# Performance work log

Hardware: AMD Instinct MI355X
Metric: run time of the kernel (lower is better)

The kernel has to match this reference:

```python
import jax, jax.numpy as jnp
import numpy as np

# Static complete 8-ary label tree, depth 4, BFS (heap) indexing:
# children of node j are 8j+1..8j+8; level d starts at (8^d - 1)/7.
BRANCH = 8
DEPTH = 4
COUNTS = [BRANCH ** d for d in range(DEPTH + 1)]   # [1, 8, 64, 512, 4096]
STARTS = np.cumsum([0] + COUNTS)[:-1]              # level start offsets
N = int(sum(COUNTS))                               # 4681 nodes
B = 64
IN_DIM = 256
MEM = 256


def setup_inputs() -> dict:
    key = jax.random.key(0)
    ks = jax.random.split(key, 8)
    def w(k, shape, fan):
        return jax.random.normal(k, shape, jnp.float32) / np.float32(np.sqrt(fan))
    return {
        "inputs": jax.random.normal(ks[0], (N, B, IN_DIM), jnp.float32),
        "prob": jax.random.uniform(ks[1], (N, N), dtype=jnp.float32),
        "Wioux": w(ks[2], (3 * MEM, IN_DIM), IN_DIM),
        "bioux": jnp.zeros((3 * MEM,), jnp.float32),
        "Wiouh": w(ks[3], (3 * MEM, MEM), MEM),
        "biouh": jnp.zeros((3 * MEM,), jnp.float32),
        "Wfx": w(ks[4], (MEM, IN_DIM), IN_DIM),
        "bfx": jnp.zeros((MEM,), jnp.float32),
        "Wfh": w(ks[5], (MEM, MEM), MEM),
        "bfh": jnp.zeros((MEM,), jnp.float32),
    }


def _linear(x, W, b):
    # torch nn.Linear: y = x @ W^T + b
    return jnp.einsum("...i,oi->...o", x, W) + b


def reference(inputs, prob, Wioux, bioux, Wiouh, biouh, Wfx, bfx, Wfh, bfh):
    # --- leaf level (deepest): child_c = child_h = 0, but iouh/fh biases still apply
    s, cnt = int(STARTS[DEPTH]), COUNTS[DEPTH]
    x = inputs[s:s + cnt]                              # [nL, B, IN]
    iou = _linear(x, Wioux, bioux) + biouh             # iouh(0) = its bias
    i, o, u = jnp.split(iou, 3, axis=-1)
    c = jax.nn.sigmoid(i) * jnp.tanh(u)                # sum(f*0) = 0 for leaves
    h = jax.nn.sigmoid(o) * jnp.tanh(c)                # [nL, B, MEM]
    # --- internal levels, bottom-up (level-synchronous == original recursion)
    for d in range(DEPTH - 1, -1, -1):
        s, cnt = int(STARTS[d]), COUNTS[d]
        parents = jnp.arange(s, s + cnt)                                   # [cnt]
        childs = BRANCH * parents[:, None] + 1 + jnp.arange(BRANCH)[None]  # [cnt,8]
        pw = prob[parents[:, None], childs]                                # [cnt,8]
        wc = pw[:, :, None, None] * c.reshape(cnt, BRANCH, B, MEM)         # weighted child_c
        wh = pw[:, :, None, None] * h.reshape(cnt, BRANCH, B, MEM)         # weighted child_h
        h_sum = wh.sum(axis=1)                                             # [cnt,B,MEM]
        x = inputs[s:s + cnt]                                              # [cnt,B,IN]
        iou = _linear(x, Wioux, bioux) + _linear(h_sum, Wiouh, biouh)
        i, o, u = jnp.split(iou, 3, axis=-1)
        f = jax.nn.sigmoid(_linear(wh, Wfh, bfh) + _linear(x, Wfx, bfx)[:, None])
        c = jax.nn.sigmoid(i) * jnp.tanh(u) + (f * wc).sum(axis=1)
        h = jax.nn.sigmoid(o) * jnp.tanh(c)
    # root bottom_up_state: (c, h), each [B, MEM]
    return c[0], h[0]
```

## Files before the change

kernel.cpp:

```cpp
#include <hip/hip_runtime.h>


typedef unsigned short u16;
typedef unsigned int u32;
typedef __bf16 bf16x8 __attribute__((ext_vector_type(8)));
typedef float f32x4 __attribute__((ext_vector_type(4)));

#define STR 72
#define NNODES 4681

__device__ __forceinline__ float bf2f(u32 lo) { return __uint_as_float(lo << 16); }
__device__ __forceinline__ u16 f2bf(float f) {
    __bf16 h = (__bf16)f;
    return *(u16*)&h;
}
__device__ __forceinline__ float rcp_(float x) { return __builtin_amdgcn_rcpf(x); }
__device__ __forceinline__ float sigm(float x) { return rcp_(1.0f + __expf(-x)); }
__device__ __forceinline__ float tanh_(float x) {
    float e = __expf(2.0f * x);
    return 1.0f - 2.0f * rcp_(e + 1.0f);
}

__device__ __forceinline__ void stage_bf16(u16* lds, const u16* src, int tid) {
    int row = tid >> 2, c = (tid & 3) * 16;
    const u16* p = src + (size_t)row * 256 + c;
    uint4 v0 = *(const uint4*)p;
    uint4 v1 = *(const uint4*)(p + 8);
    u16* q = lds + row * STR + c;
    *(uint4*)q = v0;
    *(uint4*)(q + 8) = v1;
}
__device__ __forceinline__ void stage_f32(u16* lds, const float* src, int tid) {
    int row = tid >> 2, c = (tid & 3) * 16;
    const float* p = src + (size_t)row * 256 + c;
    u16 pk[16];
#pragma unroll
    for (int q = 0; q < 4; q++) {
        float4 v = *(const float4*)(p + q * 4);
        pk[q * 4 + 0] = f2bf(v.x);
        pk[q * 4 + 1] = f2bf(v.y);
        pk[q * 4 + 2] = f2bf(v.z);
        pk[q * 4 + 3] = f2bf(v.w);
    }
    u16* q2 = lds + row * STR + c;
    *(uint4*)q2 = *(uint4*)pk;
    *(uint4*)(q2 + 8) = *(uint4*)(pk + 8);
}

template <int NG>
__device__ __forceinline__ void mma_ksub(const u16* As, const u16* Ws, int wv, int l,
                                         int s, f32x4 (*acc)[4]) {
    const int colb = l & 15, quad = l >> 4;
    const int ko = s * 32 + quad * 8;
    bf16x8 a[4];
#pragma unroll
    for (int r = 0; r < 4; r++)
        a[r] = *(const bf16x8*)(As + (r * 16 + colb) * STR + ko);
#pragma unroll
    for (int g = 0; g < NG; g++) {
        bf16x8 b = *(const bf16x8*)(Ws + g * (64 * STR) + (wv * 16 + colb) * STR + ko);
#pragma unroll
        for (int r = 0; r < 4; r++)
            acc[g][r] = __builtin_amdgcn_mfma_f32_16x16x32_bf16(a[r], b, acc[g][r], 0, 0, 0);
    }
}

__global__ __launch_bounds__(256) void k_cvtw(
    const float* __restrict__ Wioux, const float* __restrict__ Wiouh,
    const float* __restrict__ Wfx, const float* __restrict__ Wfh,
    u16* __restrict__ out) {
    int i4 = (blockIdx.x * 256 + threadIdx.x) * 4;
    const float* p;
    if (i4 < 196608) p = Wioux + i4;
    else if (i4 < 393216) p = Wiouh + (i4 - 196608);
    else if (i4 < 458752) p = Wfx + (i4 - 393216);
    else p = Wfh + (i4 - 458752);
    float4 v = *(const float4*)p;
    u16 pk[4] = {f2bf(v.x), f2bf(v.y), f2bf(v.z), f2bf(v.w)};
    *(ushort4*)(out + i4) = *(ushort4*)pk;
}

__global__ __launch_bounds__(256) void k_leaf(
    const float* __restrict__ X, const u16* __restrict__ Wxb,
    const float* __restrict__ bioux, const float* __restrict__ biouh,
    u16* __restrict__ Cp, u16* __restrict__ Hp) {
    __shared__ u16 As[64 * STR];
    __shared__ u16 Ws[3][64 * STR];
    const int tid = threadIdx.x;
    const int mem0 = blockIdx.x * 64;
    const int row0 = blockIdx.y * 64;
    const int l = tid & 63, wv = tid >> 6;
    f32x4 acc[3][4];
#pragma unroll
    for (int g = 0; g < 3; g++)
#pragma unroll
        for (int r = 0; r < 4; r++) acc[g][r] = (f32x4){0.f, 0.f, 0.f, 0.f};
    for (int kt = 0; kt < 256; kt += 64) {
        stage_f32(As, X + (size_t)row0 * 256 + kt, tid);
#pragma unroll
        for (int g = 0; g < 3; g++)
            stage_bf16(Ws[g], Wxb + ((size_t)g * 256 + mem0) * 256 + kt, tid);
        __syncthreads();
        mma_ksub<3>(As, &Ws[0][0], wv, l, 0, acc);
        mma_ksub<3>(As, &Ws[0][0], wv, l, 1, acc);
        __syncthreads();
    }
    const int colb = l & 15, quad = l >> 4;
    const int mem = mem0 + wv * 16 + colb;
    const float bi = bioux[mem] + biouh[mem];
    const float bo = bioux[256 + mem] + biouh[256 + mem];
    const float bu = bioux[512 + mem] + biouh[512 + mem];
#pragma unroll
    for (int r = 0; r < 4; r++)
#pragma unroll
        for (int reg = 0; reg < 4; reg++) {
            int row = row0 + r * 16 + quad * 4 + reg;
            float c = sigm(acc[0][r][reg] + bi) * tanh_(acc[2][r][reg] + bu);
            float h = sigm(acc[1][r][reg] + bo) * tanh_(c);
            size_t o = (size_t)row * 256 + mem;
            Cp[o] = f2bf(c);
            Hp[o] = f2bf(h);
        }
}

__global__ __launch_bounds__(256) void k_g(
    const u16* Hprev, const u16* __restrict__ Wfhb, u16* Gout) {
    __shared__ u16 As[64 * STR];
    __shared__ u16 Ws[4][64 * STR];
    const int tid = threadIdx.x;
    const int row0 = blockIdx.x * 64;
    const int l = tid & 63, wv = tid >> 6;
    f32x4 acc[4][4];
#pragma unroll
    for (int g = 0; g < 4; g++)
#pragma unroll
        for (int r = 0; r < 4; r++) acc[g][r] = (f32x4){0.f, 0.f, 0.f, 0.f};
    for (int kt = 0; kt < 256; kt += 64) {
        stage_bf16(As, Hprev + (size_t)row0 * 256 + kt, tid);
#pragma unroll
        for (int g = 0; g < 4; g++)
            stage_bf16(Ws[g], Wfhb + ((size_t)g * 64) * 256 + kt, tid);
        __syncthreads();
        mma_ksub<4>(As, &Ws[0][0], wv, l, 0, acc);
        mma_ksub<4>(As, &Ws[0][0], wv, l, 1, acc);
        __syncthreads();
    }
    const int colb = l & 15, quad = l >> 4;
#pragma unroll
    for (int g = 0; g < 4; g++)
#pragma unroll
        for (int r = 0; r < 4; r++) {
            int n = g * 64 + wv * 16 + colb;
#pragma unroll
            for (int reg = 0; reg < 4; reg++) {
                int row = row0 + r * 16 + quad * 4 + reg;
                Gout[(size_t)row * 256 + n] = f2bf(acc[g][r][reg]);
            }
        }
}

__global__ __launch_bounds__(256) void k_main(
    const float* __restrict__ X, const u16* __restrict__ Hsum,
    const u16* __restrict__ G, const u16* __restrict__ Cprev,
    const float* __restrict__ pw,
    const u16* __restrict__ Wxb, const float* __restrict__ bioux,
    const u16* __restrict__ Whb, const float* __restrict__ biouh,
    const u16* __restrict__ Wfxb, const float* __restrict__ bfx,
    const float* __restrict__ bfh,
    u16* __restrict__ Ccur, u16* __restrict__ Hcur,
    float* __restrict__ outc, float* __restrict__ outh) {
    __shared__ u16 As[64 * STR];
    __shared__ u16 Ws[4][64 * STR];
    __shared__ float pws[8];
    const int tid = threadIdx.x;
    const int mem0 = blockIdx.x * 64;
    const int lp = blockIdx.y;
    const int l = tid & 63, wv = tid >> 6;
    if (tid < 8) pws[tid] = pw[lp * 8 + tid];
    f32x4 acc[4][4];
#pragma unroll
    for (int g = 0; g < 4; g++)
#pragma unroll
        for (int r = 0; r < 4; r++) acc[g][r] = (f32x4){0.f, 0.f, 0.f, 0.f};
    for (int kt = 0; kt < 256; kt += 64) {
        stage_f32(As, X + ((size_t)lp * 64) * 256 + kt, tid);
#pragma unroll
        for (int g = 0; g < 3; g++)
            stage_bf16(Ws[g], Wxb + ((size_t)g * 256 + mem0) * 256 + kt, tid);
        stage_bf16(Ws[3], Wfxb + (size_t)mem0 * 256 + kt, tid);
        __syncthreads();
        mma_ksub<4>(As, &Ws[0][0], wv, l, 0, acc);
        mma_ksub<4>(As, &Ws[0][0], wv, l, 1, acc);
        __syncthreads();
    }
    for (int kt = 0; kt < 256; kt += 64) {
        stage_bf16(As, Hsum + ((size_t)lp * 64) * 256 + kt, tid);
#pragma unroll
        for (int g = 0; g < 3; g++)
            stage_bf16(Ws[g], Whb + ((size_t)g * 256 + mem0) * 256 + kt, tid);
        __syncthreads();
        mma_ksub<3>(As, &Ws[0][0], wv, l, 0, acc);
        mma_ksub<3>(As, &Ws[0][0], wv, l, 1, acc);
        __syncthreads();
    }
    const int colb = l & 15, quad = l >> 4;
    const int mem = mem0 + wv * 16 + colb;
    const float bi = bioux[mem] + biouh[mem];
    const float bo = bioux[256 + mem] + biouh[256 + mem];
    const float bu = bioux[512 + mem] + biouh[512 + mem];
    const float bfv = bfx[mem] + bfh[mem];
    float cac[4][4], bff[4][4], ovv[4][4];
#pragma unroll
    for (int r = 0; r < 4; r++)
#pragma unroll
        for (int reg = 0; reg < 4; reg++) {
            cac[r][reg] = sigm(acc[0][r][reg] + bi) * tanh_(acc[2][r][reg] + bu);
            ovv[r][reg] = acc[1][r][reg] + bo;
            bff[r][reg] = bfv + acc[3][r][reg];
        }
#pragma unroll
    for (int ch = 0; ch < 8; ch++) {
        float p = pws[ch];
        size_t base = (((size_t)(lp * 8 + ch) * 64) + quad * 4) * 256 + mem;
#pragma unroll
        for (int r = 0; r < 4; r++)
#pragma unroll
            for (int reg = 0; reg < 4; reg++) {
                size_t idx = base + ((size_t)r * 16 + reg) * 256;
                float gv = bf2f((u32)G[idx]);
                float cp = bf2f((u32)Cprev[idx]);
                float f = sigm(fmaf(p, gv, bff[r][reg]));
                cac[r][reg] = fmaf(f * p, cp, cac[r][reg]);
            }
    }
#pragma unroll
    for (int r = 0; r < 4; r++)
#pragma unroll
        for (int reg = 0; reg < 4; reg++) {
            int rl = r * 16 + quad * 4 + reg;
            float h = sigm(ovv[r][reg]) * tanh_(cac[r][reg]);
            size_t o = ((size_t)lp * 64 + rl) * 256 + mem;
            Ccur[o] = f2bf(cac[r][reg]);
            Hcur[o] = f2bf(h);
            if (outc) {
                size_t oo = (size_t)rl * 256 + mem;
                outc[oo] = cac[r][reg];
                outh[oo] = h;
            }
        }
}

__global__ __launch_bounds__(256) void k_hsum(
    const u16* __restrict__ Hprev, const float* __restrict__ pw,
    u16* __restrict__ Hsum, int cnt) {
    int idx = blockIdx.x * 256 + threadIdx.x;
    int total = cnt * 64 * 64;
    if (idx >= total) return;
    int q = idx & 63;
    int b = (idx >> 6) & 63;
    int lp = idx >> 12;
    float s0 = 0.f, s1 = 0.f, s2 = 0.f, s3 = 0.f;
#pragma unroll
    for (int ch = 0; ch < 8; ch++) {
        float p = pw[lp * 8 + ch];
        size_t base = (((size_t)lp * 8 + ch) * 64 + b) * 256 + q * 4;
        uint2 hh = *(const uint2*)(Hprev + base);
        s0 = fmaf(p, bf2f(hh.x & 0xffffu), s0);
        s1 = fmaf(p, bf2f(hh.x >> 16), s1);
        s2 = fmaf(p, bf2f(hh.y & 0xffffu), s2);
        s3 = fmaf(p, bf2f(hh.y >> 16), s3);
    }
    u16 pk[4] = {f2bf(s0), f2bf(s1), f2bf(s2), f2bf(s3)};
    size_t o = ((size_t)lp * 64 + b) * 256 + q * 4;
    *(ushort4*)(Hsum + o) = *(ushort4*)pk;
}

__global__ __launch_bounds__(256) void k_pw(
    const float* __restrict__ prob, float* __restrict__ pw, int s, int cnt) {
    int i = blockIdx.x * 256 + threadIdx.x;
    if (i < cnt * 8) {
        int lp = i >> 3, j = i & 7;
        int par = s + lp;
        pw[i] = prob[(size_t)par * NNODES + (8 * par + 1 + j)];
    }
}

extern "C" void kernel_launch(void* const* d_in, const int* in_sizes, int n_in,
                              void* d_out, int out_size, void* d_ws, size_t ws_size,
                              hipStream_t stream) {
    const float* inputs = (const float*)d_in[0];
    const float* prob   = (const float*)d_in[1];
    const float* Wioux  = (const float*)d_in[2];
    const float* bioux  = (const float*)d_in[3];
    const float* Wiouh  = (const float*)d_in[4];
    const float* biouh  = (const float*)d_in[5];
    const float* Wfx    = (const float*)d_in[6];
    const float* bfx    = (const float*)d_in[7];
    const float* Wfh    = (const float*)d_in[8];
    const float* bfh    = (const float*)d_in[9];
    float* outc = (float*)d_out;
    float* outh = outc + 64 * 256;

    const size_t szA = (size_t)4096 * 64 * 256 * 2;
    const size_t szB = (size_t)512 * 64 * 256 * 2;
    char* p = (char*)d_ws;
    u16* Ac = (u16*)p; p += szA;
    u16* Ah = (u16*)p; p += szA;
    u16* Bc = (u16*)p; p += szB;
    u16* Bh = (u16*)p; p += szB;
    u16* Hs = (u16*)p; p += szB;
    float* pwb = (float*)p; p += (size_t)512 * 8 * 4;
    u16* Wb = (u16*)p; p += (size_t)524288 * 2;
    u16* Wxb  = Wb;
    u16* Whb  = Wb + 196608;
    u16* Wfxb = Wb + 393216;
    u16* Wfhb = Wb + 458752;

    k_cvtw<<<512, 256, 0, stream>>>(Wioux, Wiouh, Wfx, Wfh, Wb);

    k_leaf<<<dim3(4, 4096), 256, 0, stream>>>(
        inputs + (size_t)585 * 64 * 256, Wxb, bioux, biouh, Ac, Ah);

    const int starts[4] = {0, 1, 9, 73};
    const int counts[4] = {1, 8, 64, 512};
    u16 *pc = Ac, *ph = Ah, *cc = Bc, *chh = Bh;
    for (int d = 3; d >= 0; d--) {
        int s = starts[d], cnt = counts[d];
        k_pw<<<(cnt * 8 + 255) / 256, 256, 0, stream>>>(prob, pwb, s, cnt);
        k_hsum<<<(cnt * 64 * 64 + 255) / 256, 256, 0, stream>>>(ph, pwb, Hs, cnt);
        k_g<<<cnt * 8, 256, 0, stream>>>(ph, Wfhb, ph);
        k_main<<<dim3(4, cnt), 256, 0, stream>>>(
            inputs + (size_t)s * 64 * 256, Hs, ph, pc, pwb,
            Wxb, bioux, Whb, biouh, Wfxb, bfx, bfh,
            cc, chh,
            (d == 0) ? outc : nullptr, (d == 0) ? outh : nullptr);
        u16* t;
        t = pc; pc = cc; cc = t;
        t = ph; ph = chh; chh = t;
    }
}
```

Measured before the change: 1.049 ms.

## Store weights and H as swizzled 64x64 tile images loaded directly into LDS

Weights are pre-packed into contiguous 64x64 bf16 tiles with an XOR swizzle. H activations and Hsum are written in the same tile-image layout. This lets the GEMM kernels stage operands with global_load_lds straight into LDS instead of going through registers with a padded stride, and the swizzle replaces padding to avoid LDS bank conflicts. The gain depends on correct index mapping across all producer and consumer kernels, and the fp32 X staging still goes through registers.

Measured after the change: 969.7 us. -7.5%, faster.

```diff
diff --git a/kernel.cpp b/kernel.cpp
--- a/kernel.cpp
+++ b/kernel.cpp
@@ -6,7 +6,6 @@
 typedef __bf16 bf16x8 __attribute__((ext_vector_type(8)));
 typedef float f32x4 __attribute__((ext_vector_type(4)));
 
-#define STR 72
 #define NNODES 4681
 
 __device__ __forceinline__ float bf2f(u32 lo) { return __uint_as_float(lo << 16); }
@@ -21,18 +20,23 @@
     return 1.0f - 2.0f * rcp_(e + 1.0f);
 }
 
-__device__ __forceinline__ void stage_bf16(u16* lds, const u16* src, int tid) {
-    int row = tid >> 2, c = (tid & 3) * 16;
-    const u16* p = src + (size_t)row * 256 + c;
-    uint4 v0 = *(const uint4*)p;
-    uint4 v1 = *(const uint4*)(p + 8);
-    u16* q = lds + row * STR + c;
-    *(uint4*)q = v0;
-    *(uint4*)(q + 8) = v1;
-}
-__device__ __forceinline__ void stage_f32(u16* lds, const float* src, int tid) {
-    int row = tid >> 2, c = (tid & 3) * 16;
-    const float* p = src + (size_t)row * 256 + c;
+__device__ __forceinline__ int img_off(int row, int col) {
+    return row * 64 + (((col >> 3) ^ (row & 7)) << 3) + (col & 7);
+}
+
+__device__ __forceinline__ void gll_tile(const u16* src, u16* dst, int tid) {
+    const int l = tid & 63, wv = tid >> 6;
+    const char* s = (const char*)src + wv * 2048 + l * 16;
+    char* d = (char*)dst + wv * 2048;
+    __builtin_amdgcn_global_load_lds((const __attribute__((address_space(1))) void*)s,
+                                     (__attribute__((address_space(3))) void*)d, 16, 0, 0);
+    __builtin_amdgcn_global_load_lds((const __attribute__((address_space(1))) void*)(s + 1024),
+                                     (__attribute__((address_space(3))) void*)(d + 1024), 16, 0, 0);
+}
+
+__device__ __forceinline__ void stage_f32_sw(u16* lds, const float* src, int tid) {
+    const int row = tid >> 2, c0 = (tid & 3) * 2;
+    const float* p = src + (size_t)row * 256 + (tid & 3) * 16;
     u16 pk[16];
 #pragma unroll
     for (int q = 0; q < 4; q++) {
@@ -42,23 +46,25 @@
         pk[q * 4 + 2] = f2bf(v.z);
         pk[q * 4 + 3] = f2bf(v.w);
     }
-    u16* q2 = lds + row * STR + c;
-    *(uint4*)q2 = *(uint4*)pk;
-    *(uint4*)(q2 + 8) = *(uint4*)(pk + 8);
+    const int sw = row & 7;
+    *(uint4*)(lds + row * 64 + ((c0 ^ sw) << 3)) = *(uint4*)pk;
+    *(uint4*)(lds + row * 64 + (((c0 + 1) ^ sw) << 3)) = *(uint4*)(pk + 8);
 }
 
 template <int NG>
 __device__ __forceinline__ void mma_ksub(const u16* As, const u16* Ws, int wv, int l,
                                          int s, f32x4 (*acc)[4]) {
     const int colb = l & 15, quad = l >> 4;
-    const int ko = s * 32 + quad * 8;
+    const int c = s * 4 + quad;
+    const int sc = (c ^ (colb & 7)) << 3;
     bf16x8 a[4];
 #pragma unroll
     for (int r = 0; r < 4; r++)
-        a[r] = *(const bf16x8*)(As + (r * 16 + colb) * STR + ko);
+        a[r] = *(const bf16x8*)(As + (r * 16 + colb) * 64 + sc);
+    const int boff = (wv * 16 + colb) * 64 + sc;
 #pragma unroll
     for (int g = 0; g < NG; g++) {
-        bf16x8 b = *(const bf16x8*)(Ws + g * (64 * STR) + (wv * 16 + colb) * STR + ko);
+        bf16x8 b = *(const bf16x8*)(Ws + g * 4096 + boff);
 #pragma unroll
         for (int r = 0; r < 4; r++)
             acc[g][r] = __builtin_amdgcn_mfma_f32_16x16x32_bf16(a[r], b, acc[g][r], 0, 0, 0);
@@ -69,77 +75,85 @@
     const float* __restrict__ Wioux, const float* __restrict__ Wiouh,
     const float* __restrict__ Wfx, const float* __restrict__ Wfh,
     u16* __restrict__ out) {
-    int i4 = (blockIdx.x * 256 + threadIdx.x) * 4;
-    const float* p;
-    if (i4 < 196608) p = Wioux + i4;
-    else if (i4 < 393216) p = Wiouh + (i4 - 196608);
-    else if (i4 < 458752) p = Wfx + (i4 - 393216);
-    else p = Wfh + (i4 - 458752);
-    float4 v = *(const float4*)p;
-    u16 pk[4] = {f2bf(v.x), f2bf(v.y), f2bf(v.z), f2bf(v.w)};
-    *(ushort4*)(out + i4) = *(ushort4*)pk;
+    int idx = blockIdx.x * 256 + threadIdx.x;
+    int cc5 = idx & 31, kt = cc5 >> 3, cc = cc5 & 7;
+    int rowid = idx >> 5;
+    const float* src;
+    if (rowid < 768) src = Wioux + (size_t)rowid * 256;
+    else if (rowid < 1536) src = Wiouh + (size_t)(rowid - 768) * 256;
+    else if (rowid < 1792) src = Wfx + (size_t)(rowid - 1536) * 256;
+    else src = Wfh + (size_t)(rowid - 1792) * 256;
+    src += kt * 64 + cc * 8;
+    float4 v0 = *(const float4*)src;
+    float4 v1 = *(const float4*)(src + 4);
+    u16 pk[8] = {f2bf(v0.x), f2bf(v0.y), f2bf(v0.z), f2bf(v0.w),
+                 f2bf(v1.x), f2bf(v1.y), f2bf(v1.z), f2bf(v1.w)};
+    int r = rowid & 63;
+    u16* dst = out + ((size_t)((rowid >> 6) * 4 + kt)) * 4096 + r * 64 + ((cc ^ (r & 7)) << 3);
+    *(uint4*)dst = *(uint4*)pk;
 }
 
 __global__ __launch_bounds__(256) void k_leaf(
-    const float* __restrict__ X, const u16* __restrict__ Wxb,
+    const float* __restrict__ X, const u16* __restrict__ Wp,
     const float* __restrict__ bioux, const float* __restrict__ biouh,
     u16* __restrict__ Cp, u16* __restrict__ Hp) {
-    __shared__ u16 As[64 * STR];
-    __shared__ u16 Ws[3][64 * STR];
+    __shared__ u16 As[4096];
+    __shared__ u16 Ws[3][4096];
     const int tid = threadIdx.x;
-    const int mem0 = blockIdx.x * 64;
-    const int row0 = blockIdx.y * 64;
+    const int bx = blockIdx.x;
+    const int panel = blockIdx.y;
     const int l = tid & 63, wv = tid >> 6;
     f32x4 acc[3][4];
 #pragma unroll
     for (int g = 0; g < 3; g++)
 #pragma unroll
         for (int r = 0; r < 4; r++) acc[g][r] = (f32x4){0.f, 0.f, 0.f, 0.f};
-    for (int kt = 0; kt < 256; kt += 64) {
-        stage_f32(As, X + (size_t)row0 * 256 + kt, tid);
+    for (int kt = 0; kt < 4; kt++) {
 #pragma unroll
         for (int g = 0; g < 3; g++)
-            stage_bf16(Ws[g], Wxb + ((size_t)g * 256 + mem0) * 256 + kt, tid);
+            gll_tile(Wp + ((size_t)((g * 4 + bx) * 4 + kt)) * 4096, Ws[g], tid);
+        stage_f32_sw(As, X + (size_t)panel * 16384 + kt * 64, tid);
         __syncthreads();
         mma_ksub<3>(As, &Ws[0][0], wv, l, 0, acc);
         mma_ksub<3>(As, &Ws[0][0], wv, l, 1, acc);
         __syncthreads();
     }
     const int colb = l & 15, quad = l >> 4;
-    const int mem = mem0 + wv * 16 + colb;
+    const int j = wv * 16 + colb;
+    const int mem = bx * 64 + j;
     const float bi = bioux[mem] + biouh[mem];
     const float bo = bioux[256 + mem] + biouh[256 + mem];
     const float bu = bioux[512 + mem] + biouh[512 + mem];
+    u16* Himg = Hp + ((size_t)panel * 4 + bx) * 4096;
 #pragma unroll
     for (int r = 0; r < 4; r++)
 #pragma unroll
         for (int reg = 0; reg < 4; reg++) {
-            int row = row0 + r * 16 + quad * 4 + reg;
+            int rl = r * 16 + quad * 4 + reg;
             float c = sigm(acc[0][r][reg] + bi) * tanh_(acc[2][r][reg] + bu);
             float h = sigm(acc[1][r][reg] + bo) * tanh_(c);
-            size_t o = (size_t)row * 256 + mem;
-            Cp[o] = f2bf(c);
-            Hp[o] = f2bf(h);
+            Cp[((size_t)panel * 64 + rl) * 256 + mem] = f2bf(c);
+            Himg[img_off(rl, j)] = f2bf(h);
         }
 }
 
 __global__ __launch_bounds__(256) void k_g(
-    const u16* Hprev, const u16* __restrict__ Wfhb, u16* Gout) {
-    __shared__ u16 As[64 * STR];
-    __shared__ u16 Ws[4][64 * STR];
+    const u16* Hprev, const u16* __restrict__ Wfhp, u16* Gout) {
+    __shared__ u16 As[4096];
+    __shared__ u16 Ws[4][4096];
     const int tid = threadIdx.x;
-    const int row0 = blockIdx.x * 64;
+    const int panel = blockIdx.x;
     const int l = tid & 63, wv = tid >> 6;
     f32x4 acc[4][4];
 #pragma unroll
     for (int g = 0; g < 4; g++)
 #pragma unroll
         for (int r = 0; r < 4; r++) acc[g][r] = (f32x4){0.f, 0.f, 0.f, 0.f};
-    for (int kt = 0; kt < 256; kt += 64) {
-        stage_bf16(As, Hprev + (size_t)row0 * 256 + kt, tid);
+    for (int kt = 0; kt < 4; kt++) {
+        gll_tile(Hprev + ((size_t)panel * 4 + kt) * 4096, As, tid);
 #pragma unroll
         for (int g = 0; g < 4; g++)
-            stage_bf16(Ws[g], Wfhb + ((size_t)g * 64) * 256 + kt, tid);
+            gll_tile(Wfhp + ((size_t)(g * 4 + kt)) * 4096, Ws[g], tid);
         __syncthreads();
         mma_ksub<4>(As, &Ws[0][0], wv, l, 0, acc);
         mma_ksub<4>(As, &Ws[0][0], wv, l, 1, acc);
@@ -153,7 +167,7 @@
             int n = g * 64 + wv * 16 + colb;
 #pragma unroll
             for (int reg = 0; reg < 4; reg++) {
-                int row = row0 + r * 16 + quad * 4 + reg;
+                int row = panel * 64 + r * 16 + quad * 4 + reg;
                 Gout[(size_t)row * 256 + n] = f2bf(acc[g][r][reg]);
             }
         }
@@ -163,17 +177,17 @@
     const float* __restrict__ X, const u16* __restrict__ Hsum,
     const u16* __restrict__ G, const u16* __restrict__ Cprev,
     const float* __restrict__ pw,
-    const u16* __restrict__ Wxb, const float* __restrict__ bioux,
-    const u16* __restrict__ Whb, const float* __restrict__ biouh,
-    const u16* __restrict__ Wfxb, const float* __restrict__ bfx,
+    const u16* __restrict__ Wxp, const float* __restrict__ bioux,
+    const u16* __restrict__ Whp, const float* __restrict__ biouh,
+    const u16* __restrict__ Wfxp, const float* __restrict__ bfx,
     const float* __restrict__ bfh,
     u16* __restrict__ Ccur, u16* __restrict__ Hcur,
     float* __restrict__ outc, float* __restrict__ outh) {
-    __shared__ u16 As[64 * STR];
-    __shared__ u16 Ws[4][64 * STR];
+    __shared__ u16 As[4096];
+    __shared__ u16 Ws[4][4096];
     __shared__ float pws[8];
     const int tid = threadIdx.x;
-    const int mem0 = blockIdx.x * 64;
+    const int bx = blockIdx.x;
     const int lp = blockIdx.y;
     const int l = tid & 63, wv = tid >> 6;
     if (tid < 8) pws[tid] = pw[lp * 8 + tid];
@@ -182,29 +196,30 @@
     for (int g = 0; g < 4; g++)
 #pragma unroll
         for (int r = 0; r < 4; r++) acc[g][r] = (f32x4){0.f, 0.f, 0.f, 0.f};
-    for (int kt = 0; kt < 256; kt += 64) {
-        stage_f32(As, X + ((size_t)lp * 64) * 256 + kt, tid);
+    for (int kt = 0; kt < 4; kt++) {
 #pragma unroll
         for (int g = 0; g < 3; g++)
-            stage_bf16(Ws[g], Wxb + ((size_t)g * 256 + mem0) * 256 + kt, tid);
-        stage_bf16(Ws[3], Wfxb + (size_t)mem0 * 256 + kt, tid);
+            gll_tile(Wxp + ((size_t)((g * 4 + bx) * 4 + kt)) * 4096, Ws[g], tid);
+        gll_tile(Wfxp + ((size_t)(bx * 4 + kt)) * 4096, Ws[3], tid);
+        stage_f32_sw(As, X + (size_t)lp * 16384 + kt * 64, tid);
         __syncthreads();
         mma_ksub<4>(As, &Ws[0][0], wv, l, 0, acc);
         mma_ksub<4>(As, &Ws[0][0], wv, l, 1, acc);
         __syncthreads();
     }
-    for (int kt = 0; kt < 256; kt += 64) {
-        stage_bf16(As, Hsum + ((size_t)lp * 64) * 256 + kt, tid);
+    for (int kt = 0; kt < 4; kt++) {
+        gll_tile(Hsum + ((size_t)lp * 4 + kt) * 4096, As, tid);
 #pragma unroll
         for (int g = 0; g < 3; g++)
-            stage_bf16(Ws[g], Whb + ((size_t)g * 256 + mem0) * 256 + kt, tid);
+            gll_tile(Whp + ((size_t)((g * 4 + bx) * 4 + kt)) * 4096, Ws[g], tid);
         __syncthreads();
         mma_ksub<3>(As, &Ws[0][0], wv, l, 0, acc);
         mma_ksub<3>(As, &Ws[0][0], wv, l, 1, acc);
         __syncthreads();
     }
     const int colb = l & 15, quad = l >> 4;
-    const int mem = mem0 + wv * 16 + colb;
+    const int j = wv * 16 + colb;
+    const int mem = bx * 64 + j;
     const float bi = bioux[mem] + biouh[mem];
     const float bo = bioux[256 + mem] + biouh[256 + mem];
     const float bu = bioux[512 + mem] + biouh[512 + mem];
@@ -233,15 +248,15 @@
                 cac[r][reg] = fmaf(f * p, cp, cac[r][reg]);
             }
     }
+    u16* Himg = Hcur + ((size_t)lp * 4 + bx) * 4096;
 #pragma unroll
     for (int r = 0; r < 4; r++)
 #pragma unroll
         for (int reg = 0; reg < 4; reg++) {
             int rl = r * 16 + quad * 4 + reg;
             float h = sigm(ovv[r][reg]) * tanh_(cac[r][reg]);
-            size_t o = ((size_t)lp * 64 + rl) * 256 + mem;
-            Ccur[o] = f2bf(cac[r][reg]);
-            Hcur[o] = f2bf(h);
+            Ccur[((size_t)lp * 64 + rl) * 256 + mem] = f2bf(cac[r][reg]);
+            Himg[img_off(rl, j)] = f2bf(h);
             if (outc) {
                 size_t oo = (size_t)rl * 256 + mem;
                 outc[oo] = cac[r][reg];
@@ -254,25 +269,31 @@
     const u16* __restrict__ Hprev, const float* __restrict__ pw,
     u16* __restrict__ Hsum, int cnt) {
     int idx = blockIdx.x * 256 + threadIdx.x;
-    int total = cnt * 64 * 64;
-    if (idx >= total) return;
-    int q = idx & 63;
-    int b = (idx >> 6) & 63;
-    int lp = idx >> 12;
-    float s0 = 0.f, s1 = 0.f, s2 = 0.f, s3 = 0.f;
+    if (idx >= cnt * 64 * 32) return;
+    int cc5 = idx & 31, kt = cc5 >> 3, cc = cc5 & 7;
+    int b = (idx >> 5) & 63;
+    int lp = idx >> 11;
+    const int off = b * 64 + ((cc ^ (b & 7)) << 3);
+    float s[8] = {0.f, 0.f, 0.f, 0.f, 0.f, 0.f, 0.f, 0.f};
 #pragma unroll
     for (int ch = 0; ch < 8; ch++) {
         float p = pw[lp * 8 + ch];
-        size_t base = (((size_t)lp * 8 + ch) * 64 + b) * 256 + q * 4;
-        uint2 hh = *(const uint2*)(Hprev + base);
-        s0 = fmaf(p, bf2f(hh.x & 0xffffu), s0);
-        s1 = fmaf(p, bf2f(hh.x >> 16), s1);
-        s2 = fmaf(p, bf2f(hh.y & 0xffffu), s2);
-        s3 = fmaf(p, bf2f(hh.y >> 16), s3);
-    }
-    u16 pk[4] = {f2bf(s0), f2bf(s1), f2bf(s2), f2bf(s3)};
-    size_t o = ((size_t)lp * 64 + b) * 256 + q * 4;
-    *(ushort4*)(Hsum + o) = *(ushort4*)pk;
+        const u16* src = Hprev + ((size_t)(lp * 8 + ch) * 4 + kt) * 4096 + off;
+        uint4 hh = *(const uint4*)src;
+        s[0] = fmaf(p, bf2f(hh.x & 0xffffu), s[0]);
+        s[1] = fmaf(p, bf2f(hh.x >> 16), s[1]);
+        s[2] = fmaf(p, bf2f(hh.y & 0xffffu), s[2]);
+        s[3] = fmaf(p, bf2f(hh.y >> 16), s[3]);
+        s[4] = fmaf(p, bf2f(hh.z & 0xffffu), s[4]);
+        s[5] = fmaf(p, bf2f(hh.z >> 16), s[5]);
+        s[6] = fmaf(p, bf2f(hh.w & 0xffffu), s[6]);
+        s[7] = fmaf(p, bf2f(hh.w >> 16), s[7]);
+    }
+    u16 pk[8];
+#pragma unroll
+    for (int i = 0; i < 8; i++) pk[i] = f2bf(s[i]);
+    u16* dst = Hsum + ((size_t)lp * 4 + kt) * 4096 + off;
+    *(uint4*)dst = *(uint4*)pk;
 }
 
 __global__ __launch_bounds__(256) void k_pw(
@@ -310,16 +331,16 @@
     u16* Bh = (u16*)p; p += szB;
     u16* Hs = (u16*)p; p += szB;
     float* pwb = (float*)p; p += (size_t)512 * 8 * 4;
-    u16* Wb = (u16*)p; p += (size_t)524288 * 2;
-    u16* Wxb  = Wb;
-    u16* Whb  = Wb + 196608;
-    u16* Wfxb = Wb + 393216;
-    u16* Wfhb = Wb + 458752;
-
-    k_cvtw<<<512, 256, 0, stream>>>(Wioux, Wiouh, Wfx, Wfh, Wb);
+    u16* Wb = (u16*)p; p += (size_t)32 * 4 * 4096 * 2;
+    u16* Wxp  = Wb;
+    u16* Whp  = Wb + 196608;
+    u16* Wfxp = Wb + 393216;
+    u16* Wfhp = Wb + 458752;
+
+    k_cvtw<<<256, 256, 0, stream>>>(Wioux, Wiouh, Wfx, Wfh, Wb);
 
     k_leaf<<<dim3(4, 4096), 256, 0, stream>>>(
-        inputs + (size_t)585 * 64 * 256, Wxb, bioux, biouh, Ac, Ah);
+        inputs + (size_t)585 * 64 * 256, Wxp, bioux, biouh, Ac, Ah);
 
     const int starts[4] = {0, 1, 9, 73};
     const int counts[4] = {1, 8, 64, 512};
@@ -327,11 +348,11 @@
     for (int d = 3; d >= 0; d--) {
         int s = starts[d], cnt = counts[d];
         k_pw<<<(cnt * 8 + 255) / 256, 256, 0, stream>>>(prob, pwb, s, cnt);
-        k_hsum<<<(cnt * 64 * 64 + 255) / 256, 256, 0, stream>>>(ph, pwb, Hs, cnt);
-        k_g<<<cnt * 8, 256, 0, stream>>>(ph, Wfhb, ph);
+        k_hsum<<<cnt * 8, 256, 0, stream>>>(ph, pwb, Hs, cnt);
+        k_g<<<cnt * 8, 256, 0, stream>>>(ph, Wfhp, ph);
         k_main<<<dim3(4, cnt), 256, 0, stream>>>(
             inputs + (size_t)s * 64 * 256, Hs, ph, pc, pwb,
-            Wxb, bioux, Whb, biouh, Wfxb, bfx, bfh,
+            Wxp, bioux, Whp, biouh, Wfxp, bfx, bfh,
             cc, chh,
             (d == 0) ? outc : nullptr, (d == 0) ? outh : nullptr);
         u16* t;
```
